# Kernel tuning notes

Measured on AMD Instinct MI355X. Metric: run time of the kernel, lower is better.

Reference implementation:

```python
import jax, jax.numpy as jnp
import numpy as np

IN_C, OUT_C, K = 32, 32, 3
PAD = 1


def setup_inputs() -> dict:
    key = jax.random.key(0)
    kx, kw, kb = jax.random.split(key, 3)
    x = jax.random.normal(kx, (16, IN_C, 256, 256), dtype=jnp.float32)
    # Kaiming-ish init scale for the conv weight, matching nn.Conv2d defaults roughly
    fan_in = IN_C * K * K
    w = jax.random.normal(kw, (OUT_C, IN_C, K, K), dtype=jnp.float32) / np.sqrt(fan_in)
    b = jax.random.normal(kb, (OUT_C,), dtype=jnp.float32) * 0.01
    return {"x": x, "weight": w, "bias": b}


def reference(x, weight, bias):
    # Faithful math of SparseConv2d.forward: the block-sparse Triton path computes
    # the same result as a dense conv (zero blocks contribute zero), so the
    # reference is a standard 3x3 stride-1 pad-1 conv, NCHW / OIHW layout.
    y = jax.lax.conv_general_dilated(
        x, weight,
        window_strides=(1, 1),
        padding=((PAD, PAD), (PAD, PAD)),
        dimension_numbers=("NCHW", "OIHW", "NCHW"),
    )
    return y + bias[None, :, None, None]
```

## Files before the change

kernel.cpp:

```cpp
#include <hip/hip_runtime.h>


constexpr int N_  = 16;
constexpr int C_  = 32;
constexpr int OC_ = 32;
constexpr int H_  = 256;
constexpr int W_  = 256;

constexpr int XSTR = 20;
constexpr int XROW = 258 * XSTR;
constexpr int WSTRD = 36;
constexpr int WELEMS = 9 * 32 * WSTRD;
constexpr int WBYTES = WELEMS * 2;

typedef __attribute__((ext_vector_type(4)))  short short4v;
typedef __attribute__((ext_vector_type(8)))  short short8v;
typedef __attribute__((ext_vector_type(16))) float float16v;

static __device__ __forceinline__ unsigned short f2bf(float f) {
    unsigned int u = __float_as_uint(f);
    unsigned int r = (u + 0x7FFFu + ((u >> 16) & 1u)) >> 16;
    return (unsigned short)r;
}

static __device__ __forceinline__ unsigned cvtpk(float lo, float hi) {
    unsigned r;
    asm("v_cvt_pk_bf16_f32 %0, %1, %2" : "=v"(r) : "v"(lo), "v"(hi));
    return r;
}

static __device__ __forceinline__ short8v load8(const unsigned short* p) {
    short4v lo = *(const short4v*)p;
    short4v hi = *(const short4v*)(p + 4);
    return __builtin_shufflevector(lo, hi, 0, 1, 2, 3, 4, 5, 6, 7);
}

__global__ void conv_w_prep(const float* __restrict__ wgt,
                            unsigned short* __restrict__ wp) {
    const int i = blockIdx.x * 256 + threadIdx.x;
    if (i >= OC_ * C_ * 9) return;
    const float v = wgt[i];
    const int oc  = i / 288;
    const int rem = i - oc * 288;
    const int ic  = rem / 9;
    const int t9  = rem - ic * 9;
    wp[(t9 * 32 + oc) * WSTRD + ic] = f2bf(v);
}

template<bool USE_WS>
__global__ __launch_bounds__(512, 4) void conv3x3_mfma_kernel(
    const float* __restrict__ x,
    const float* __restrict__ wgt,
    const float* __restrict__ bias,
    const unsigned short* __restrict__ wpk,
    float* __restrict__ out)
{
    __shared__ __align__(16) unsigned short ldsX[4 * XROW];
    __shared__ __align__(16) unsigned short ldsW[WELEMS];

    const int tid = threadIdx.x;

    const int id = blockIdx.x;
    const int L  = (id & 7) * 256 + (id >> 3);
    const int n  = L >> 7;
    const int h  = (L & 127) * 2;

    const int lane = tid & 63;
    const int wv   = tid >> 6;
    const int rsel = wv >> 2;
    const int col  = lane & 31;
    const int qd   = lane >> 5;
    const int w0a  = (wv & 3) * 64;
    const int w0b  = (wv & 3) * 64 + 32;

    const int r4  = tid >> 7;
    const int t7  = tid & 127;
    const int wlo = t7 & 31;
    const int icq = t7 >> 5;
    const size_t HW = (size_t)H_ * W_;

    float2 a0[4], a1[4], b0r[4], b1r[4];
    auto load_half = [&](int half) {
        const int icg0 = half * 16 + 2 * icq;
        const int icg1 = half * 16 + 2 * (icq + 4);
        const int hy = h - 1 + r4;
        if (hy >= 0 && hy < H_) {
            const float* pA0 = x + ((size_t)(n * C_ + icg0) * H_ + hy) * W_;
            const float* pA1 = pA0 + HW;
            const float* pB0 = x + ((size_t)(n * C_ + icg1) * H_ + hy) * W_;
            const float* pB1 = pB0 + HW;
            #pragma unroll
            for (int wb = 0; wb < 4; ++wb) {
                const int w = wb * 64 + 2 * wlo;
                a0[wb]  = *(const float2*)(pA0 + w);
                a1[wb]  = *(const float2*)(pA1 + w);
                b0r[wb] = *(const float2*)(pB0 + w);
                b1r[wb] = *(const float2*)(pB1 + w);
            }
        } else {
            #pragma unroll
            for (int wb = 0; wb < 4; ++wb) {
                a0[wb] = a1[wb] = b0r[wb] = b1r[wb] = make_float2(0.f, 0.f);
            }
        }
    };
    load_half(0);

    if (USE_WS) {
        const int4* src = (const int4*)wpk;
        int4* dstW = (int4*)&ldsW[0];
        #pragma unroll
        for (int i2 = 0; i2 < 3; ++i2) {
            const int idx = tid + i2 * 512;
            if (idx < WBYTES / 16) dstW[idx] = src[idx];
        }
    } else {
        for (int i = tid; i < OC_ * C_ * 9; i += 512) {
            const float v = wgt[i];
            const int oc  = i / 288;
            const int rem = i - oc * 288;
            const int ic  = rem / 9;
            const int t9  = rem - ic * 9;
            ldsW[(t9 * 32 + oc) * WSTRD + ic] = f2bf(v);
        }
    }

    float16v acc0, acc1;
    #pragma unroll
    for (int r = 0; r < 16; ++r) {
        const float bv = bias[(r & 3) + 8 * (r >> 2) + 4 * qd];
        acc0[r] = bv;
        acc1[r] = bv;
    }

    auto write_half = [&]() {
        unsigned short* dst = &ldsX[r4 * XROW];
        #pragma unroll
        for (int wb = 0; wb < 4; ++wb) {
            const int w = wb * 64 + 2 * wlo;
            *(unsigned*)&dst[(w + 1) * XSTR + 2 * icq]       = cvtpk(a0[wb].x,  a1[wb].x);
            *(unsigned*)&dst[(w + 2) * XSTR + 2 * icq]       = cvtpk(a0[wb].y,  a1[wb].y);
            *(unsigned*)&dst[(w + 1) * XSTR + 2 * (icq + 4)] = cvtpk(b0r[wb].x, b1r[wb].x);
            *(unsigned*)&dst[(w + 2) * XSTR + 2 * (icq + 4)] = cvtpk(b0r[wb].y, b1r[wb].y);
        }
    };

    auto mfma_half = [&](int half) {
        #pragma unroll
        for (int kh = 0; kh < 3; ++kh) {
            #pragma unroll
            for (int kw = 0; kw < 3; ++kw) {
                const int t9 = kh * 3 + kw;
                const short8v av =
                    load8(&ldsW[(t9 * 32 + col) * WSTRD + half * 16 + qd * 8]);
                const short8v bf0 =
                    load8(&ldsX[(rsel + kh) * XROW + (w0a + col + kw) * XSTR + qd * 8]);
                const short8v bf1 =
                    load8(&ldsX[(rsel + kh) * XROW + (w0b + col + kw) * XSTR + qd * 8]);
                acc0 = __builtin_amdgcn_mfma_f32_32x32x16_bf16(av, bf0, acc0, 0, 0, 0);
                acc1 = __builtin_amdgcn_mfma_f32_32x32x16_bf16(av, bf1, acc1, 0, 0, 0);
            }
        }
    };

    write_half();
    if (tid < 32) {
        const int r  = tid >> 3;
        const int q  = tid & 7;
        const int wi = (q & 4) ? 257 : 0;
        const int c  = q & 3;
        *(unsigned long long*)&ldsX[r * XROW + wi * XSTR + c * 4] = 0ull;
    }
    __syncthreads();

    load_half(1);
    mfma_half(0);
    __syncthreads();

    write_half();
    __syncthreads();
    mfma_half(1);

    float* outp = out + (size_t)n * OC_ * HW + (size_t)(h + rsel) * W_;
    #pragma unroll
    for (int r = 0; r < 16; ++r) {
        const int oc = (r & 3) + 8 * (r >> 2) + 4 * qd;
        __builtin_nontemporal_store(acc0[r], &outp[(size_t)oc * HW + w0a + col]);
        __builtin_nontemporal_store(acc1[r], &outp[(size_t)oc * HW + w0b + col]);
    }
}

extern "C" void kernel_launch(void* const* d_in, const int* in_sizes, int n_in,
                              void* d_out, int out_size, void* d_ws, size_t ws_size,
                              hipStream_t stream) {
    const float* x    = (const float*)d_in[0];
    const float* wgt  = (const float*)d_in[1];
    const float* bias = (const float*)d_in[2];
    float* out        = (float*)d_out;

    dim3 grid(N_ * H_ / 2);
    dim3 block(512);

    if (d_ws != nullptr && ws_size >= (size_t)WBYTES) {
        unsigned short* wp = (unsigned short*)d_ws;
        conv_w_prep<<<dim3(36), dim3(256), 0, stream>>>(wgt, wp);
        conv3x3_mfma_kernel<true><<<grid, block, 0, stream>>>(x, wgt, bias, wp, out);
    } else {
        conv3x3_mfma_kernel<false><<<grid, block, 0, stream>>>(x, wgt, bias, nullptr, out);
    }
}
```

Baseline: 243.3 us.

## Process eight output rows per block with rolling three-row LDS input buffer

Each block now computes 8 consecutive output rows instead of 2. It keeps a circular 3-row LDS buffer holding all 32 input channels and streams in one new input row per iteration, so each input row is loaded and converted about once rather than re-read for every row pair, and the weight load is amortised over more work. Half of the A fragments stay in registers across iterations. The cost is fewer blocks (512), two barriers per row, more registers, and less overlap between global loads and MFMA inside each block.

```diff
diff --git a/kernel.cpp b/kernel.cpp
--- a/kernel.cpp
+++ b/kernel.cpp
@@ -7,7 +7,8 @@
 constexpr int H_  = 256;
 constexpr int W_  = 256;
 
-constexpr int XSTR = 20;
+constexpr int ROWS = 8;
+constexpr int XSTR = 36;
 constexpr int XROW = 258 * XSTR;
 constexpr int WSTRD = 36;
 constexpr int WELEMS = 9 * 32 * WSTRD;
@@ -55,56 +56,79 @@
     const unsigned short* __restrict__ wpk,
     float* __restrict__ out)
 {
-    __shared__ __align__(16) unsigned short ldsX[4 * XROW];
+    __shared__ __align__(16) unsigned short ldsX[3 * XROW];
     __shared__ __align__(16) unsigned short ldsW[WELEMS];
 
     const int tid = threadIdx.x;
 
     const int id = blockIdx.x;
-    const int L  = (id & 7) * 256 + (id >> 3);
-    const int n  = L >> 7;
-    const int h  = (L & 127) * 2;
+    const int L  = (id & 7) * 64 + (id >> 3);
+    const int n  = L >> 5;
+    const int h0 = (L & 31) * ROWS;
 
     const int lane = tid & 63;
     const int wv   = tid >> 6;
-    const int rsel = wv >> 2;
     const int col  = lane & 31;
     const int qd   = lane >> 5;
-    const int w0a  = (wv & 3) * 64;
-    const int w0b  = (wv & 3) * 64 + 32;
-
-    const int r4  = tid >> 7;
-    const int t7  = tid & 127;
-    const int wlo = t7 & 31;
-    const int icq = t7 >> 5;
+    const int w0   = wv * 32;
+
+    const int wlo = tid & 31;
+    const int icp = tid >> 5;
     const size_t HW = (size_t)H_ * W_;
 
-    float2 a0[4], a1[4], b0r[4], b1r[4];
-    auto load_half = [&](int half) {
-        const int icg0 = half * 16 + 2 * icq;
-        const int icg1 = half * 16 + 2 * (icq + 4);
-        const int hy = h - 1 + r4;
+    const float* xrow0 = x + (size_t)(n * C_ + 2 * icp) * HW;
+    const float* xrow1 = xrow0 + HW;
+
+    float2 ra[4], rb[4];
+    auto load_row = [&](int hy) {
         if (hy >= 0 && hy < H_) {
-            const float* pA0 = x + ((size_t)(n * C_ + icg0) * H_ + hy) * W_;
-            const float* pA1 = pA0 + HW;
-            const float* pB0 = x + ((size_t)(n * C_ + icg1) * H_ + hy) * W_;
-            const float* pB1 = pB0 + HW;
+            const float* p0 = xrow0 + (size_t)hy * W_;
+            const float* p1 = xrow1 + (size_t)hy * W_;
             #pragma unroll
             for (int wb = 0; wb < 4; ++wb) {
                 const int w = wb * 64 + 2 * wlo;
-                a0[wb]  = *(const float2*)(pA0 + w);
-                a1[wb]  = *(const float2*)(pA1 + w);
-                b0r[wb] = *(const float2*)(pB0 + w);
-                b1r[wb] = *(const float2*)(pB1 + w);
+                ra[wb] = *(const float2*)(p0 + w);
+                rb[wb] = *(const float2*)(p1 + w);
             }
         } else {
             #pragma unroll
             for (int wb = 0; wb < 4; ++wb) {
-                a0[wb] = a1[wb] = b0r[wb] = b1r[wb] = make_float2(0.f, 0.f);
+                ra[wb] = make_float2(0.f, 0.f);
+                rb[wb] = make_float2(0.f, 0.f);
             }
         }
     };
-    load_half(0);
+    auto write_row = [&](int slot) {
+        unsigned short* dst = &ldsX[slot * XROW];
+        #pragma unroll
+        for (int wb = 0; wb < 4; ++wb) {
+            const int w = wb * 64 + 2 * wlo;
+            *(unsigned*)&dst[(w + 1) * XSTR + 2 * icp] = cvtpk(ra[wb].x, rb[wb].x);
+            *(unsigned*)&dst[(w + 2) * XSTR + 2 * icp] = cvtpk(ra[wb].y, rb[wb].y);
+        }
+    };
+
+    float2 qa[3][4], qb[3][4];
+    #pragma unroll
+    for (int rr = 0; rr < 3; ++rr) {
+        const int hy = h0 - 1 + rr;
+        if (hy >= 0 && hy < H_) {
+            const float* p0 = xrow0 + (size_t)hy * W_;
+            const float* p1 = xrow1 + (size_t)hy * W_;
+            #pragma unroll
+            for (int wb = 0; wb < 4; ++wb) {
+                const int w = wb * 64 + 2 * wlo;
+                qa[rr][wb] = *(const float2*)(p0 + w);
+                qb[rr][wb] = *(const float2*)(p1 + w);
+            }
+        } else {
+            #pragma unroll
+            for (int wb = 0; wb < 4; ++wb) {
+                qa[rr][wb] = make_float2(0.f, 0.f);
+                qb[rr][wb] = make_float2(0.f, 0.f);
+            }
+        }
+    }
 
     if (USE_WS) {
         const int4* src = (const int4*)wpk;
@@ -125,68 +149,71 @@
         }
     }
 
-    float16v acc0, acc1;
-    #pragma unroll
-    for (int r = 0; r < 16; ++r) {
-        const float bv = bias[(r & 3) + 8 * (r >> 2) + 4 * qd];
-        acc0[r] = bv;
-        acc1[r] = bv;
-    }
-
-    auto write_half = [&]() {
-        unsigned short* dst = &ldsX[r4 * XROW];
+    #pragma unroll
+    for (int rr = 0; rr < 3; ++rr) {
+        unsigned short* dst = &ldsX[rr * XROW];
         #pragma unroll
         for (int wb = 0; wb < 4; ++wb) {
             const int w = wb * 64 + 2 * wlo;
-            *(unsigned*)&dst[(w + 1) * XSTR + 2 * icq]       = cvtpk(a0[wb].x,  a1[wb].x);
-            *(unsigned*)&dst[(w + 2) * XSTR + 2 * icq]       = cvtpk(a0[wb].y,  a1[wb].y);
-            *(unsigned*)&dst[(w + 1) * XSTR + 2 * (icq + 4)] = cvtpk(b0r[wb].x, b1r[wb].x);
-            *(unsigned*)&dst[(w + 2) * XSTR + 2 * (icq + 4)] = cvtpk(b0r[wb].y, b1r[wb].y);
-        }
-    };
-
-    auto mfma_half = [&](int half) {
+            *(unsigned*)&dst[(w + 1) * XSTR + 2 * icp] = cvtpk(qa[rr][wb].x, qb[rr][wb].x);
+            *(unsigned*)&dst[(w + 2) * XSTR + 2 * icp] = cvtpk(qa[rr][wb].y, qb[rr][wb].y);
+        }
+    }
+    if (tid < 108) {
+        const int slot = tid / 36;
+        const int q    = tid - slot * 36;
+        const int wi   = (q >= 18) ? 257 : 0;
+        const int dw   = (q >= 18) ? q - 18 : q;
+        ((unsigned*)&ldsX[slot * XROW + wi * XSTR])[dw] = 0u;
+    }
+    __syncthreads();
+
+    short8v a0f[9];
+    #pragma unroll
+    for (int t9 = 0; t9 < 9; ++t9)
+        a0f[t9] = load8(&ldsW[(t9 * 32 + col) * WSTRD + qd * 8]);
+    float bv[16];
+    #pragma unroll
+    for (int r = 0; r < 16; ++r)
+        bv[r] = bias[(r & 3) + 8 * (r >> 2) + 4 * qd];
+
+    #pragma unroll
+    for (int it = 0; it < ROWS; ++it) {
+        const int h = h0 + it;
+        const bool stg = (it < ROWS - 1);
+        if (stg) load_row(h + 2);
+
+        float16v acc;
+        #pragma unroll
+        for (int r = 0; r < 16; ++r) acc[r] = bv[r];
+
         #pragma unroll
         for (int kh = 0; kh < 3; ++kh) {
+            const unsigned short* bb = &ldsX[((it + kh) % 3) * XROW];
             #pragma unroll
             for (int kw = 0; kw < 3; ++kw) {
                 const int t9 = kh * 3 + kw;
-                const short8v av =
-                    load8(&ldsW[(t9 * 32 + col) * WSTRD + half * 16 + qd * 8]);
-                const short8v bf0 =
-                    load8(&ldsX[(rsel + kh) * XROW + (w0a + col + kw) * XSTR + qd * 8]);
-                const short8v bf1 =
-                    load8(&ldsX[(rsel + kh) * XROW + (w0b + col + kw) * XSTR + qd * 8]);
-                acc0 = __builtin_amdgcn_mfma_f32_32x32x16_bf16(av, bf0, acc0, 0, 0, 0);
-                acc1 = __builtin_amdgcn_mfma_f32_32x32x16_bf16(av, bf1, acc1, 0, 0, 0);
-            }
-        }
-    };
-
-    write_half();
-    if (tid < 32) {
-        const int r  = tid >> 3;
-        const int q  = tid & 7;
-        const int wi = (q & 4) ? 257 : 0;
-        const int c  = q & 3;
-        *(unsigned long long*)&ldsX[r * XROW + wi * XSTR + c * 4] = 0ull;
-    }
-    __syncthreads();
-
-    load_half(1);
-    mfma_half(0);
-    __syncthreads();
-
-    write_half();
-    __syncthreads();
-    mfma_half(1);
-
-    float* outp = out + (size_t)n * OC_ * HW + (size_t)(h + rsel) * W_;
-    #pragma unroll
-    for (int r = 0; r < 16; ++r) {
-        const int oc = (r & 3) + 8 * (r >> 2) + 4 * qd;
-        __builtin_nontemporal_store(acc0[r], &outp[(size_t)oc * HW + w0a + col]);
-        __builtin_nontemporal_store(acc1[r], &outp[(size_t)oc * HW + w0b + col]);
+                const int wi = w0 + col + kw;
+                const short8v b0 = load8(&bb[wi * XSTR + qd * 8]);
+                acc = __builtin_amdgcn_mfma_f32_32x32x16_bf16(a0f[t9], b0, acc, 0, 0, 0);
+                const short8v a1 = load8(&ldsW[(t9 * 32 + col) * WSTRD + 16 + qd * 8]);
+                const short8v b1 = load8(&bb[wi * XSTR + 16 + qd * 8]);
+                acc = __builtin_amdgcn_mfma_f32_32x32x16_bf16(a1, b1, acc, 0, 0, 0);
+            }
+        }
+
+        float* outp = out + (size_t)n * OC_ * HW + (size_t)h * W_;
+        #pragma unroll
+        for (int r = 0; r < 16; ++r) {
+            const int oc = (r & 3) + 8 * (r >> 2) + 4 * qd;
+            __builtin_nontemporal_store(acc[r], &outp[(size_t)oc * HW + w0 + col]);
+        }
+
+        if (stg) {
+            __syncthreads();
+            write_row(it % 3);
+            __syncthreads();
+        }
     }
 }
 
@@ -198,7 +225,7 @@
     const float* bias = (const float*)d_in[2];
     float* out        = (float*)d_out;
 
-    dim3 grid(N_ * H_ / 2);
+    dim3 grid(N_ * H_ / ROWS);
     dim3 block(512);
 
     if (d_ws != nullptr && ws_size >= (size_t)WBYTES) {
```

Result: slower. 286.1 us (+17.6%).

## Process four row-pair tiles per block with software-pipelined global loads

Applied to the files above, without the earlier changes.

Each block now walks four consecutive two-row output tiles instead of one. The packed weights in LDS and the block setup are reused across tiles, and the next tile's input half is prefetched into registers while the current tile's MFMAs run. Barriers become explicit lgkmcnt waits plus s_barrier. The grid shrinks by four, which trades parallelism and occupancy for better amortization, and the halo rows are still reloaded for each tile.

```diff
diff --git a/kernel.cpp b/kernel.cpp
--- a/kernel.cpp
+++ b/kernel.cpp
@@ -7,6 +7,7 @@
 constexpr int H_  = 256;
 constexpr int W_  = 256;
 
+constexpr int TILES = 4;
 constexpr int XSTR = 20;
 constexpr int XROW = 258 * XSTR;
 constexpr int WSTRD = 36;
@@ -33,6 +34,12 @@
     short4v lo = *(const short4v*)p;
     short4v hi = *(const short4v*)(p + 4);
     return __builtin_shufflevector(lo, hi, 0, 1, 2, 3, 4, 5, 6, 7);
+}
+
+static __device__ __forceinline__ void bar_lgkm() {
+    asm volatile("s_waitcnt lgkmcnt(0)" ::: "memory");
+    __builtin_amdgcn_s_barrier();
+    __builtin_amdgcn_sched_barrier(0);
 }
 
 __global__ void conv_w_prep(const float* __restrict__ wgt,
@@ -61,9 +68,9 @@
     const int tid = threadIdx.x;
 
     const int id = blockIdx.x;
-    const int L  = (id & 7) * 256 + (id >> 3);
-    const int n  = L >> 7;
-    const int h  = (L & 127) * 2;
+    const int L  = (id & 7) * 64 + (id >> 3);
+    const int n  = L >> 5;
+    const int h0 = (L & 31) * 8;
 
     const int lane = tid & 63;
     const int wv   = tid >> 6;
@@ -80,10 +87,10 @@
     const size_t HW = (size_t)H_ * W_;
 
     float2 a0[4], a1[4], b0r[4], b1r[4];
-    auto load_half = [&](int half) {
-        const int icg0 = half * 16 + 2 * icq;
-        const int icg1 = half * 16 + 2 * (icq + 4);
-        const int hy = h - 1 + r4;
+    auto load_stage = [&](int t, int hf) {
+        const int icg0 = hf * 16 + 2 * icq;
+        const int icg1 = hf * 16 + 2 * (icq + 4);
+        const int hy = h0 + 2 * t - 1 + r4;
         if (hy >= 0 && hy < H_) {
             const float* pA0 = x + ((size_t)(n * C_ + icg0) * H_ + hy) * W_;
             const float* pA1 = pA0 + HW;
@@ -104,7 +111,19 @@
             }
         }
     };
-    load_half(0);
+    auto write_stage = [&]() {
+        unsigned short* dst = &ldsX[r4 * XROW];
+        #pragma unroll
+        for (int wb = 0; wb < 4; ++wb) {
+            const int w = wb * 64 + 2 * wlo;
+            *(unsigned*)&dst[(w + 1) * XSTR + 2 * icq]       = cvtpk(a0[wb].x,  a1[wb].x);
+            *(unsigned*)&dst[(w + 2) * XSTR + 2 * icq]       = cvtpk(a0[wb].y,  a1[wb].y);
+            *(unsigned*)&dst[(w + 1) * XSTR + 2 * (icq + 4)] = cvtpk(b0r[wb].x, b1r[wb].x);
+            *(unsigned*)&dst[(w + 2) * XSTR + 2 * (icq + 4)] = cvtpk(b0r[wb].y, b1r[wb].y);
+        }
+    };
+
+    load_stage(0, 0);
 
     if (USE_WS) {
         const int4* src = (const int4*)wpk;
@@ -125,45 +144,12 @@
         }
     }
 
-    float16v acc0, acc1;
+    float16v accb;
     #pragma unroll
-    for (int r = 0; r < 16; ++r) {
-        const float bv = bias[(r & 3) + 8 * (r >> 2) + 4 * qd];
-        acc0[r] = bv;
-        acc1[r] = bv;
-    }
-
-    auto write_half = [&]() {
-        unsigned short* dst = &ldsX[r4 * XROW];
-        #pragma unroll
-        for (int wb = 0; wb < 4; ++wb) {
-            const int w = wb * 64 + 2 * wlo;
-            *(unsigned*)&dst[(w + 1) * XSTR + 2 * icq]       = cvtpk(a0[wb].x,  a1[wb].x);
-            *(unsigned*)&dst[(w + 2) * XSTR + 2 * icq]       = cvtpk(a0[wb].y,  a1[wb].y);
-            *(unsigned*)&dst[(w + 1) * XSTR + 2 * (icq + 4)] = cvtpk(b0r[wb].x, b1r[wb].x);
-            *(unsigned*)&dst[(w + 2) * XSTR + 2 * (icq + 4)] = cvtpk(b0r[wb].y, b1r[wb].y);
-        }
-    };
-
-    auto mfma_half = [&](int half) {
-        #pragma unroll
-        for (int kh = 0; kh < 3; ++kh) {
-            #pragma unroll
-            for (int kw = 0; kw < 3; ++kw) {
-                const int t9 = kh * 3 + kw;
-                const short8v av =
-                    load8(&ldsW[(t9 * 32 + col) * WSTRD + half * 16 + qd * 8]);
-                const short8v bf0 =
-                    load8(&ldsX[(rsel + kh) * XROW + (w0a + col + kw) * XSTR + qd * 8]);
-                const short8v bf1 =
-                    load8(&ldsX[(rsel + kh) * XROW + (w0b + col + kw) * XSTR + qd * 8]);
-                acc0 = __builtin_amdgcn_mfma_f32_32x32x16_bf16(av, bf0, acc0, 0, 0, 0);
-                acc1 = __builtin_amdgcn_mfma_f32_32x32x16_bf16(av, bf1, acc1, 0, 0, 0);
-            }
-        }
-    };
-
-    write_half();
+    for (int r = 0; r < 16; ++r)
+        accb[r] = bias[(r & 3) + 8 * (r >> 2) + 4 * qd];
+
+    write_stage();
     if (tid < 32) {
         const int r  = tid >> 3;
         const int q  = tid & 7;
@@ -171,22 +157,53 @@
         const int c  = q & 3;
         *(unsigned long long*)&ldsX[r * XROW + wi * XSTR + c * 4] = 0ull;
     }
-    __syncthreads();
-
-    load_half(1);
-    mfma_half(0);
-    __syncthreads();
-
-    write_half();
-    __syncthreads();
-    mfma_half(1);
-
-    float* outp = out + (size_t)n * OC_ * HW + (size_t)(h + rsel) * W_;
+    load_stage(0, 1);
+    bar_lgkm();
+
+    auto mfma_half = [&](int hf, float16v& c0, float16v& c1) {
+        #pragma unroll
+        for (int kh = 0; kh < 3; ++kh) {
+            #pragma unroll
+            for (int kw = 0; kw < 3; ++kw) {
+                const int t9 = kh * 3 + kw;
+                const short8v av =
+                    load8(&ldsW[(t9 * 32 + col) * WSTRD + hf * 16 + qd * 8]);
+                const short8v bf0 =
+                    load8(&ldsX[(rsel + kh) * XROW + (w0a + col + kw) * XSTR + qd * 8]);
+                const short8v bf1 =
+                    load8(&ldsX[(rsel + kh) * XROW + (w0b + col + kw) * XSTR + qd * 8]);
+                c0 = __builtin_amdgcn_mfma_f32_32x32x16_bf16(av, bf0, c0, 0, 0, 0);
+                c1 = __builtin_amdgcn_mfma_f32_32x32x16_bf16(av, bf1, c1, 0, 0, 0);
+            }
+        }
+    };
+
     #pragma unroll
-    for (int r = 0; r < 16; ++r) {
-        const int oc = (r & 3) + 8 * (r >> 2) + 4 * qd;
-        __builtin_nontemporal_store(acc0[r], &outp[(size_t)oc * HW + w0a + col]);
-        __builtin_nontemporal_store(acc1[r], &outp[(size_t)oc * HW + w0b + col]);
+    for (int t = 0; t < TILES; ++t) {
+        float16v acc0 = accb, acc1 = accb;
+
+        mfma_half(0, acc0, acc1);
+        bar_lgkm();
+        write_stage();
+        bar_lgkm();
+
+        if (t < TILES - 1) load_stage(t + 1, 0);
+        mfma_half(1, acc0, acc1);
+
+        float* outp = out + (size_t)n * OC_ * HW + (size_t)(h0 + 2 * t + rsel) * W_;
+        #pragma unroll
+        for (int r = 0; r < 16; ++r) {
+            const int oc = (r & 3) + 8 * (r >> 2) + 4 * qd;
+            __builtin_nontemporal_store(acc0[r], &outp[(size_t)oc * HW + w0a + col]);
+            __builtin_nontemporal_store(acc1[r], &outp[(size_t)oc * HW + w0b + col]);
+        }
+
+        if (t < TILES - 1) {
+            bar_lgkm();
+            write_stage();
+            load_stage(t + 1, 1);
+            bar_lgkm();
+        }
     }
 }
 
@@ -198,7 +215,7 @@
     const float* bias = (const float*)d_in[2];
     float* out        = (float*)d_out;
 
-    dim3 grid(N_ * H_ / 2);
+    dim3 grid(N_ * H_ / (2 * TILES));
     dim3 block(512);
 
     if (d_ws != nullptr && ws_size >= (size_t)WBYTES) {
```

Result: slower. 306.3 us (+25.9%).
